# Performance work log

Measured on AMD Instinct MI355X. Metric: run time of the kernel, lower is better.

Reference implementation:

```python
import jax, jax.numpy as jnp
import numpy as np

D_MODEL = 768
BOTTLENECK = 64
LN_EPS = 1e-5
SCALE = 1.0


def setup_inputs() -> dict:
    key = jax.random.key(0)
    k_x, k_wd = jax.random.split(key, 2)
    x = jax.random.normal(k_x, (8, 4096, D_MODEL), dtype=jnp.float32)
    # LayerNorm params (torch default init: weight=1, bias=0)
    ln_w = jnp.ones((D_MODEL,), dtype=jnp.float32)
    ln_b = jnp.zeros((D_MODEL,), dtype=jnp.float32)
    # down_proj: kaiming_uniform(a=sqrt(5)) -> bound = 1/sqrt(fan_in)
    bound = 1.0 / np.sqrt(D_MODEL)
    w_down = jax.random.uniform(k_wd, (BOTTLENECK, D_MODEL), dtype=jnp.float32,
                                minval=-bound, maxval=bound)
    b_down = jnp.zeros((BOTTLENECK,), dtype=jnp.float32)
    # up_proj initialized to zeros per the module; use small random values
    # instead so the backward test is non-degenerate? No: stay faithful but
    # zeros would kill gradients through w_down; use a tiny random up matrix
    # (mathematically same op, just different param values).
    k_wu = jax.random.fold_in(key, 7)
    w_up = 0.02 * jax.random.normal(k_wu, (D_MODEL, BOTTLENECK), dtype=jnp.float32)
    b_up = jnp.zeros((D_MODEL,), dtype=jnp.float32)
    return {"x": x, "ln_w": ln_w, "ln_b": ln_b,
            "w_down": w_down, "b_down": b_down,
            "w_up": w_up, "b_up": b_up}


def reference(x, ln_w, ln_b, w_down, b_down, w_up, b_up):
    # adapter_layernorm_option == 'in': LayerNorm first
    mu = jnp.mean(x, axis=-1, keepdims=True)
    var = jnp.mean(jnp.square(x - mu), axis=-1, keepdims=True)
    xn = (x - mu) * jax.lax.rsqrt(var + LN_EPS) * ln_w + ln_b
    # down projection + ReLU (dropout p=0 in eval -> identity)
    down = jax.nn.relu(jnp.einsum('bsd,kd->bsk', xn, w_down) + b_down)
    # up projection, scale, residual add (add_residual=True, residual=x)
    up = (jnp.einsum('bsk,dk->bsd', down, w_up) + b_up) * SCALE
    return up + x
```

## Files before the change

### kernel.cpp

```cpp
#include <hip/hip_runtime.h>

#define D_MODEL 768
#define BN 64
#define LN_EPS 1e-5f
#define MFMA __builtin_amdgcn_mfma_f32_16x16x32_bf16

typedef __attribute__((ext_vector_type(8))) short bf16x8;
typedef __attribute__((ext_vector_type(4))) float f32x4;

static __device__ __forceinline__ unsigned short f2bf(float f) {
    unsigned int u = __float_as_uint(f);
    u = (u + 0x7FFFu + ((u >> 16) & 1u)) >> 16;
    return (unsigned short)u;
}
static __device__ __forceinline__ float bf2f(unsigned short u) {
    return __uint_as_float(((unsigned int)u) << 16);
}

__global__ void prep(const float* __restrict__ wd, const float* __restrict__ ln_w,
                     const float* __restrict__ ln_b, const float* __restrict__ b_down,
                     const float* __restrict__ wu,
                     unsigned short* __restrict__ wd2_frag, unsigned short* __restrict__ wu_frag,
                     float* __restrict__ S, float* __restrict__ bd2) {
    const int b = blockIdx.x;
    const int t = threadIdx.x;
    const int c = b;
    const int wv = c >> 4, cl = c & 15;
    float s = 0.f, sb = 0.f;
    #pragma unroll
    for (int i = 0; i < 12; ++i) {
        const int d = t + 64 * i;
        const float w0 = wd[c * D_MODEL + d];
        const float w2 = w0 * ln_w[d];
        s  += w2;
        sb += w0 * ln_b[d];
        const int ks = d >> 5, kg = (d >> 3) & 3, e = d & 7;
        wd2_frag[(((wv * 24 + ks) * 64) + kg * 16 + cl) * 8 + e] = f2bf(w2);
    }
    #pragma unroll
    for (int off = 1; off < 64; off <<= 1) {
        s  += __shfl_xor(s, off);
        sb += __shfl_xor(sb, off);
    }
    if (t == 0) { S[c] = s; bd2[c] = b_down[c] + sb; }
    #pragma unroll
    for (int i = 0; i < 12; ++i) {
        const int n = b * 12 + i;
        const float v = wu[n * BN + t];
        const int jj = n >> 4, nl = n & 15;
        const int h = t >> 5, kg = (t >> 3) & 3, e = t & 7;
        wu_frag[(((jj * 2 + h) * 64) + kg * 16 + nl) * 8 + e] = f2bf(v);
    }
}

__global__ __launch_bounds__(256, 4) void adapter_kernel(
    const float* __restrict__ x,
    const unsigned short* __restrict__ wd2_frag, const float* __restrict__ S,
    const float* __restrict__ bd2,
    const unsigned short* __restrict__ wu_frag, const float* __restrict__ b_up,
    float* __restrict__ out)
{
    __shared__ __align__(16) unsigned short sX[16 * 768];
    __shared__ __align__(16) unsigned short sDown[16][72];
    __shared__ float sMu[16], sRs[16];

    const int tid  = threadIdx.x;
    const int lane = tid & 63;
    const int w    = tid >> 6;
    const int kg   = lane >> 4;
    const int l16  = lane & 15;
    const size_t gt0 = (size_t)blockIdx.x * 16;

    const int c = w * 16 + l16;
    const float Sc = S[c], bd = bd2[c];

    const unsigned short* bp = wd2_frag + ((size_t)(w * 24) * 64 + lane) * 8;
    bf16x8 bq[6];
    {
        float4 v[12];
        const float* base0 = x + (gt0 + (size_t)(w * 4)) * D_MODEL + lane * 4;
        #pragma unroll
        for (int p = 0; p < 4; ++p)
            #pragma unroll
            for (int sg = 0; sg < 3; ++sg)
                v[p * 3 + sg] = *(const float4*)(base0 + p * D_MODEL + sg * 256);
        #pragma unroll
        for (int i = 0; i < 6; ++i) bq[i] = *(const bf16x8*)(bp + i * 512);

        #pragma unroll
        for (int p = 0; p < 4; ++p) {
            const int r = w * 4 + p;
            float sum = 0.f, sq = 0.f;
            #pragma unroll
            for (int sg = 0; sg < 3; ++sg) {
                const float4 f = v[p * 3 + sg];
                sum += (f.x + f.y) + (f.z + f.w);
                sq  += (f.x * f.x + f.y * f.y) + (f.z * f.z + f.w * f.w);
            }
            #pragma unroll
            for (int off = 1; off < 64; off <<= 1) {
                sum += __shfl_xor(sum, off);
                sq  += __shfl_xor(sq, off);
            }
            if (lane == 0) {
                const float mu = sum * (1.f / D_MODEL);
                sMu[r] = mu;
                sRs[r] = rsqrtf(sq * (1.f / D_MODEL) - mu * mu + LN_EPS);
            }
            #pragma unroll
            for (int sg = 0; sg < 3; ++sg) {
                const float4 f = v[p * 3 + sg];
                ushort4 o;
                o.x = f2bf(f.x); o.y = f2bf(f.y); o.z = f2bf(f.z); o.w = f2bf(f.w);
                const int bytecol = ((sg * 256 + lane * 4) * 2) ^ ((r & 15) << 4);
                *(ushort4*)((char*)sX + r * 1536 + bytecol) = o;
            }
        }
    }
    __syncthreads();

    {
        const char* sxrow = (const char*)sX + l16 * 1536;
        f32x4 acc = {0.f, 0.f, 0.f, 0.f};
        #pragma unroll
        for (int ks = 0; ks < 24; ++ks) {
            const bf16x8 a = *(const bf16x8*)(sxrow + ((ks * 64 + kg * 16) ^ (l16 << 4)));
            const bf16x8 b = bq[ks % 6];
            if (ks + 6 < 24) bq[ks % 6] = *(const bf16x8*)(bp + (ks + 6) * 512);
            acc = MFMA(a, b, acc, 0, 0, 0);
        }
        #pragma unroll
        for (int r = 0; r < 4; ++r) {
            const int t = kg * 4 + r;
            const float vv = sRs[t] * (acc[r] - sMu[t] * Sc) + bd;
            sDown[t][c] = f2bf(vv > 0.f ? vv : 0.f);
        }
    }
    bf16x8 aq0[3], aq1[3];
    #pragma unroll
    for (int i = 0; i < 3; ++i) {
        const unsigned short* ap = wu_frag + ((size_t)((4 * i + w) * 2) * 64 + lane) * 8;
        aq0[i] = *(const bf16x8*)ap;
        aq1[i] = *(const bf16x8*)(ap + 512);
    }
    __syncthreads();

    {
        const bf16x8 pb0 = *(const bf16x8*)&sDown[l16][kg * 8];
        const bf16x8 pb1 = *(const bf16x8*)&sDown[l16][32 + kg * 8];
        const size_t rowOff = (gt0 + l16) * D_MODEL;
        const char* sxrow = (const char*)sX + l16 * 1536;
        #pragma unroll
        for (int j = 0; j < 12; ++j) {
            const int jj = 4 * j + w;
            const bf16x8 a0 = aq0[j % 3];
            const bf16x8 a1 = aq1[j % 3];
            if (j + 3 < 12) {
                const unsigned short* ap = wu_frag + ((size_t)((4 * (j + 3) + w) * 2) * 64 + lane) * 8;
                aq0[j % 3] = *(const bf16x8*)ap;
                aq1[j % 3] = *(const bf16x8*)(ap + 512);
            }
            f32x4 acc = {0.f, 0.f, 0.f, 0.f};
            acc = MFMA(a0, pb0, acc, 0, 0, 0);
            acc = MFMA(a1, pb1, acc, 0, 0, 0);
            const int oc = jj * 16 + kg * 4;
            const float4 bu = *(const float4*)(b_up + oc);
            const ushort4 xb = *(const ushort4*)(sxrow + ((oc * 2) ^ (l16 << 4)));
            f32x4 o;
            o[0] = acc[0] + bu.x + bf2f(xb.x);
            o[1] = acc[1] + bu.y + bf2f(xb.y);
            o[2] = acc[2] + bu.z + bf2f(xb.z);
            o[3] = acc[3] + bu.w + bf2f(xb.w);
            __builtin_nontemporal_store(o, (f32x4*)(out + rowOff + oc));
        }
    }
}

extern "C" void kernel_launch(void* const* d_in, const int* in_sizes, int n_in,
                              void* d_out, int out_size, void* d_ws, size_t ws_size,
                              hipStream_t stream) {
    const float* x      = (const float*)d_in[0];
    const float* ln_w   = (const float*)d_in[1];
    const float* ln_b   = (const float*)d_in[2];
    const float* w_down = (const float*)d_in[3];
    const float* b_down = (const float*)d_in[4];
    const float* w_up   = (const float*)d_in[5];
    const float* b_up   = (const float*)d_in[6];
    float* out = (float*)d_out;

    unsigned short* wd2_frag = (unsigned short*)d_ws;
    unsigned short* wu_frag  = wd2_frag + BN * D_MODEL;
    float* S   = (float*)((char*)d_ws + 2 * BN * D_MODEL * sizeof(unsigned short));
    float* bd2 = S + BN;

    prep<<<BN, 64, 0, stream>>>(w_down, ln_w, ln_b, b_down, w_up, wd2_frag, wu_frag, S, bd2);

    const int tokens = in_sizes[0] / D_MODEL;
    const int grid = tokens / 16;
    adapter_kernel<<<grid, 256, 0, stream>>>(x, wd2_frag, S, bd2, wu_frag, b_up, out);
}
```

Before: 52.57 us.

## Process 32 tokens per block to reuse weight fragments across two row tiles

Each block now handles 32 tokens instead of 16. Every weight fragment loaded for the down and up projections feeds two MFMAs, one per 16-row tile, which halves weight reloads per token and halves the grid size. LDS use doubles to about 50KB per block, which can reduce occupancy, and the output stores switch from nontemporal to regular stores.

```diff
diff --git a/kernel.cpp b/kernel.cpp
--- a/kernel.cpp
+++ b/kernel.cpp
@@ -60,36 +60,39 @@
     const unsigned short* __restrict__ wu_frag, const float* __restrict__ b_up,
     float* __restrict__ out)
 {
-    __shared__ __align__(16) unsigned short sX[16 * 768];
-    __shared__ __align__(16) unsigned short sDown[16][72];
-    __shared__ float sMu[16], sRs[16];
+    __shared__ __align__(16) unsigned short sX[32 * 768];
+    __shared__ __align__(16) unsigned short sDown[32][72];
+    __shared__ float sMu[32], sRs[32];
 
     const int tid  = threadIdx.x;
     const int lane = tid & 63;
     const int w    = tid >> 6;
     const int kg   = lane >> 4;
     const int l16  = lane & 15;
-    const size_t gt0 = (size_t)blockIdx.x * 16;
+    const size_t gt0 = (size_t)blockIdx.x * 32;
 
     const int c = w * 16 + l16;
     const float Sc = S[c], bd = bd2[c];
 
     const unsigned short* bp = wd2_frag + ((size_t)(w * 24) * 64 + lane) * 8;
     bf16x8 bq[6];
-    {
+
+    #pragma unroll
+    for (int p4 = 0; p4 < 2; ++p4) {
         float4 v[12];
-        const float* base0 = x + (gt0 + (size_t)(w * 4)) * D_MODEL + lane * 4;
+        const float* base0 = x + (gt0 + (size_t)(w * 8 + p4 * 4)) * D_MODEL + lane * 4;
         #pragma unroll
         for (int p = 0; p < 4; ++p)
             #pragma unroll
             for (int sg = 0; sg < 3; ++sg)
                 v[p * 3 + sg] = *(const float4*)(base0 + p * D_MODEL + sg * 256);
-        #pragma unroll
-        for (int i = 0; i < 6; ++i) bq[i] = *(const bf16x8*)(bp + i * 512);
-
+        if (p4 == 0) {
+            #pragma unroll
+            for (int i = 0; i < 6; ++i) bq[i] = *(const bf16x8*)(bp + i * 512);
+        }
         #pragma unroll
         for (int p = 0; p < 4; ++p) {
-            const int r = w * 4 + p;
+            const int r = w * 8 + p4 * 4 + p;
             float sum = 0.f, sq = 0.f;
             #pragma unroll
             for (int sg = 0; sg < 3; ++sg) {
@@ -120,20 +123,27 @@
     __syncthreads();
 
     {
-        const char* sxrow = (const char*)sX + l16 * 1536;
-        f32x4 acc = {0.f, 0.f, 0.f, 0.f};
+        const char* sxrow0 = (const char*)sX + l16 * 1536;
+        const char* sxrow1 = (const char*)sX + (16 + l16) * 1536;
+        f32x4 acc0 = {0.f, 0.f, 0.f, 0.f}, acc1 = {0.f, 0.f, 0.f, 0.f};
         #pragma unroll
         for (int ks = 0; ks < 24; ++ks) {
-            const bf16x8 a = *(const bf16x8*)(sxrow + ((ks * 64 + kg * 16) ^ (l16 << 4)));
+            const int off = (ks * 64 + kg * 16) ^ (l16 << 4);
+            const bf16x8 a0 = *(const bf16x8*)(sxrow0 + off);
+            const bf16x8 a1 = *(const bf16x8*)(sxrow1 + off);
             const bf16x8 b = bq[ks % 6];
             if (ks + 6 < 24) bq[ks % 6] = *(const bf16x8*)(bp + (ks + 6) * 512);
-            acc = MFMA(a, b, acc, 0, 0, 0);
+            acc0 = MFMA(a0, b, acc0, 0, 0, 0);
+            acc1 = MFMA(a1, b, acc1, 0, 0, 0);
         }
         #pragma unroll
         for (int r = 0; r < 4; ++r) {
-            const int t = kg * 4 + r;
-            const float vv = sRs[t] * (acc[r] - sMu[t] * Sc) + bd;
-            sDown[t][c] = f2bf(vv > 0.f ? vv : 0.f);
+            const int t0 = kg * 4 + r;
+            const float v0 = sRs[t0] * (acc0[r] - sMu[t0] * Sc) + bd;
+            sDown[t0][c] = f2bf(v0 > 0.f ? v0 : 0.f);
+            const int t1 = 16 + kg * 4 + r;
+            const float v1 = sRs[t1] * (acc1[r] - sMu[t1] * Sc) + bd;
+            sDown[t1][c] = f2bf(v1 > 0.f ? v1 : 0.f);
         }
     }
     bf16x8 aq0[3], aq1[3];
@@ -146,10 +156,14 @@
     __syncthreads();
 
     {
-        const bf16x8 pb0 = *(const bf16x8*)&sDown[l16][kg * 8];
-        const bf16x8 pb1 = *(const bf16x8*)&sDown[l16][32 + kg * 8];
-        const size_t rowOff = (gt0 + l16) * D_MODEL;
-        const char* sxrow = (const char*)sX + l16 * 1536;
+        const bf16x8 pb0_0 = *(const bf16x8*)&sDown[l16][kg * 8];
+        const bf16x8 pb1_0 = *(const bf16x8*)&sDown[l16][32 + kg * 8];
+        const bf16x8 pb0_1 = *(const bf16x8*)&sDown[16 + l16][kg * 8];
+        const bf16x8 pb1_1 = *(const bf16x8*)&sDown[16 + l16][32 + kg * 8];
+        const size_t rowOff0 = (gt0 + l16) * D_MODEL;
+        const size_t rowOff1 = (gt0 + 16 + l16) * D_MODEL;
+        const char* sxrow0 = (const char*)sX + l16 * 1536;
+        const char* sxrow1 = (const char*)sX + (16 + l16) * 1536;
         #pragma unroll
         for (int j = 0; j < 12; ++j) {
             const int jj = 4 * j + w;
@@ -160,18 +174,31 @@
                 aq0[j % 3] = *(const bf16x8*)ap;
                 aq1[j % 3] = *(const bf16x8*)(ap + 512);
             }
-            f32x4 acc = {0.f, 0.f, 0.f, 0.f};
-            acc = MFMA(a0, pb0, acc, 0, 0, 0);
-            acc = MFMA(a1, pb1, acc, 0, 0, 0);
             const int oc = jj * 16 + kg * 4;
             const float4 bu = *(const float4*)(b_up + oc);
-            const ushort4 xb = *(const ushort4*)(sxrow + ((oc * 2) ^ (l16 << 4)));
-            f32x4 o;
-            o[0] = acc[0] + bu.x + bf2f(xb.x);
-            o[1] = acc[1] + bu.y + bf2f(xb.y);
-            o[2] = acc[2] + bu.z + bf2f(xb.z);
-            o[3] = acc[3] + bu.w + bf2f(xb.w);
-            __builtin_nontemporal_store(o, (f32x4*)(out + rowOff + oc));
+            const int xoff = (oc * 2) ^ (l16 << 4);
+
+            f32x4 accA = {0.f, 0.f, 0.f, 0.f};
+            accA = MFMA(a0, pb0_0, accA, 0, 0, 0);
+            accA = MFMA(a1, pb1_0, accA, 0, 0, 0);
+            const ushort4 xb0 = *(const ushort4*)(sxrow0 + xoff);
+            float4 o0;
+            o0.x = accA[0] + bu.x + bf2f(xb0.x);
+            o0.y = accA[1] + bu.y + bf2f(xb0.y);
+            o0.z = accA[2] + bu.z + bf2f(xb0.z);
+            o0.w = accA[3] + bu.w + bf2f(xb0.w);
+            *(float4*)(out + rowOff0 + oc) = o0;
+
+            f32x4 accB = {0.f, 0.f, 0.f, 0.f};
+            accB = MFMA(a0, pb0_1, accB, 0, 0, 0);
+            accB = MFMA(a1, pb1_1, accB, 0, 0, 0);
+            const ushort4 xb1 = *(const ushort4*)(sxrow1 + xoff);
+            float4 o1;
+            o1.x = accB[0] + bu.x + bf2f(xb1.x);
+            o1.y = accB[1] + bu.y + bf2f(xb1.y);
+            o1.z = accB[2] + bu.z + bf2f(xb1.z);
+            o1.w = accB[3] + bu.w + bf2f(xb1.w);
+            *(float4*)(out + rowOff1 + oc) = o1;
         }
     }
 }
@@ -196,6 +223,6 @@
     prep<<<BN, 64, 0, stream>>>(w_down, ln_w, ln_b, b_down, w_up, wd2_frag, wu_frag, S, bd2);
 
     const int tokens = in_sizes[0] / D_MODEL;
-    const int grid = tokens / 16;
+    const int grid = tokens / 32;
     adapter_kernel<<<grid, 256, 0, stream>>>(x, wd2_frag, S, bd2, wu_frag, b_up, out);
 }
```

Result: faster. 49.91 us (-5.1%).
